# Kernel optimization log

Hardware: AMD Instinct MI355X
Metric: run time of the kernel (lower is better)

The kernel has to match this reference:

```python
import jax, jax.numpy as jnp
import numpy as np

SR = 24000          # sampling_rate
MAX_H = 60          # min(n_harmonics=100, 60)


def _interp_linear(x, T):
    """Linear upsample along axis 1, align_corners=True. x: [B, C, F] -> [B, T, F]."""
    B, C, F = x.shape
    src = jnp.arange(T, dtype=x.dtype) * ((C - 1) / (T - 1))
    i0 = jnp.clip(jnp.floor(src).astype(jnp.int32), 0, C - 2)
    frac = (src - i0.astype(x.dtype))[None, :, None]
    return x[:, i0, :] * (1.0 - frac) + x[:, i0 + 1, :] * frac


def setup_inputs() -> dict:
    key = jax.random.key(0)
    k1, k2, k3, k4, k5 = jax.random.split(key, 5)
    B, T, H, C, NF = 8, 48000, MAX_H, 100, 5
    f0 = 100.0 + 300.0 * jax.random.uniform(k1, (B, T, 1), dtype=jnp.float32)
    amplitudes = jax.random.uniform(k2, (B, T, H), dtype=jnp.float32)
    formant_freqs = 200.0 + 3300.0 * jax.random.uniform(k3, (B, C, NF), dtype=jnp.float32)
    formant_bws = 50.0 + 150.0 * jax.random.uniform(k4, (B, C, NF), dtype=jnp.float32)
    formant_amps = jax.random.uniform(k5, (B, C, NF), dtype=jnp.float32)
    initial_phase = jnp.zeros((B, 1, 1), dtype=jnp.float32)
    return {"f0": f0, "amplitudes": amplitudes, "formant_freqs": formant_freqs,
            "formant_bws": formant_bws, "formant_amps": formant_amps,
            "initial_phase": initial_phase}


def reference(f0, amplitudes, formant_freqs, formant_bws, formant_amps, initial_phase):
    B, T, _ = f0.shape
    f0 = jax.lax.stop_gradient(f0)                    # torch: f0.detach()
    voiced = (f0[..., 0] > 0).astype(f0.dtype)        # [B, T]
    phase = jnp.cumsum(2.0 * np.pi * f0 / SR, axis=1) + initial_phase  # [B, T, 1]

    ff = _interp_linear(formant_freqs, T)             # [B, T, NF]
    fb = _interp_linear(formant_bws, T)
    fa = _interp_linear(formant_amps, T)

    h = jnp.arange(1, MAX_H + 1, dtype=f0.dtype)      # [H]
    h_freq = f0 * h                                   # [B, T, H]
    nyq = (h_freq < SR / 2).astype(f0.dtype)          # [B, T, H]

    # formant resonance factor: prod over formants of (1 + amp*bw^2/((h_freq-freq)^2+bw^2))
    factor = jnp.ones_like(h_freq)
    for f in range(ff.shape[-1]):                     # NF = 5, small fixed loop
        freq = ff[:, :, f:f + 1]
        bw = fb[:, :, f:f + 1]
        amp = fa[:, :, f:f + 1]
        factor = factor * (1.0 + amp * bw * bw / ((h_freq - freq) ** 2 + bw * bw))

    osc = jnp.sin(phase * h)                          # [B, T, H]
    signal = jnp.sum(osc * amplitudes * factor * nyq, axis=-1) * voiced  # [B, T]

    final_phase = jax.lax.stop_gradient(phase[:, -1:, :] % (2.0 * np.pi))  # [B, 1, 1]
    return signal, final_phase
```

## Files before the change

kernel.cpp:

```cpp
#include <hip/hip_runtime.h>
#include <math.h>

#define SRATE   24000.0
#define NB      8
#define NT      48000
#define NH      60
#define NC      100
#define NFMT    5
#define CTS     64
#define NCH     (NT / CTS)
#define TWO_PI  6.283185307179586476925286766559

typedef float v2f __attribute__((ext_vector_type(2)));

__global__ __launch_bounds__(256) void k_partial(const float* __restrict__ f0,
                                                 double* __restrict__ part) {
    int b = blockIdx.y;
    int ch = blockIdx.x * 4 + (threadIdx.x >> 6);
    int lane = threadIdx.x & 63;
    if (ch < NCH) {
        int t = ch * CTS + lane;
        double q = (double)f0[b * NT + t];
        #pragma unroll
        for (int off = 32; off > 0; off >>= 1)
            q += __shfl_down(q, off, 64);
        if (lane == 0) part[b * NCH + ch] = q;
    }
}

__global__ __launch_bounds__(256) void k_scan(const double* __restrict__ part,
                                              double* __restrict__ offs,
                                              const float* __restrict__ initp,
                                              float* __restrict__ outf) {
    int b = blockIdx.x;
    int tid = threadIdx.x;
    int lane = tid & 63, wv = tid >> 6;
    int base = tid * 3;
    double v0 = (base     < NCH) ? part[b * NCH + base    ] : 0.0;
    double v1 = (base + 1 < NCH) ? part[b * NCH + base + 1] : 0.0;
    double v2 = (base + 2 < NCH) ? part[b * NCH + base + 2] : 0.0;
    double s = v0 + v1 + v2;
    double inc = s;
    #pragma unroll
    for (int off = 1; off < 64; off <<= 1) {
        double n = __shfl_up(inc, off, 64);
        if (lane >= off) inc += n;
    }
    __shared__ double wtot[4];
    if (lane == 63) wtot[wv] = inc;
    __syncthreads();
    double woff = 0.0;
    #pragma unroll
    for (int w = 0; w < 4; ++w)
        if (w < wv) woff += wtot[w];
    double excl = woff + inc - s;
    if (base     < NCH) offs[b * NCH + base    ] = excl;
    if (base + 1 < NCH) offs[b * NCH + base + 1] = excl + v0;
    if (base + 2 < NCH) offs[b * NCH + base + 2] = excl + v0 + v1;
    if (tid == 255) {
        double carry = woff + inc;
        double rev = carry * (1.0 / SRATE) + (double)initp[b] * (1.0 / TWO_PI);
        double fr = rev - floor(rev);
        outf[b] = (float)(fr * TWO_PI);
    }
}

__global__ __launch_bounds__(256) void k_main(const float* __restrict__ f0,
                                              const float* __restrict__ amps,
                                              const float* __restrict__ ffq,
                                              const float* __restrict__ fbw,
                                              const float* __restrict__ fam,
                                              const float* __restrict__ initp,
                                              const double* __restrict__ offs,
                                              float* __restrict__ out) {
    int b = blockIdx.y, ch = blockIdx.x;
    int wv   = threadIdx.x >> 6;
    int lane = threadIdx.x & 63;
    int g = wv * 16 + (lane >> 2);
    int j = lane & 3;
    int t_pre = ch * CTS + lane;
    int t_g   = ch * CTS + g;

    float f0v = f0[b * NT + t_pre];
    float f0s = f0v * (1.0f / 256.0f);
    float f0s_g = __shfl(f0s, g, 64);

    const float4* row = (const float4*)(amps + ((size_t)b * NT + (size_t)t_g) * NH);
    float4 q[4];
    q[0] = row[j];
    q[1] = row[4 + j];
    q[2] = make_float4(0.f, 0.f, 0.f, 0.f);
    q[3] = make_float4(0.f, 0.f, 0.f, 0.f);
    if (f0s_g * 33.0f < 46.875f) q[2] = row[8 + j];
    if (j < 3 && f0s_g * 49.0f < 46.875f) q[3] = row[12 + j];

    double inc = (double)f0v;
    #pragma unroll
    for (int off = 1; off < 64; off <<= 1) {
        double n = __shfl_up(inc, off, 64);
        if (lane >= off) inc += n;
    }
    double pre = offs[b * NCH + ch];
    double rev = (pre + inc) * (1.0 / SRATE) + (double)initp[b] * (1.0 / TWO_PI);
    float rev_f = (float)(rev - floor(rev));
    float rev_g = __shfl(rev_f, g, 64);

    double srcd = (double)t_g * (99.0 / 47999.0);
    int i0 = (int)srcd;
    if (i0 > NC - 2) i0 = NC - 2;
    float frac = (float)(srcd - (double)i0);
    float omf = 1.0f - frac;
    const float* Fq = ffq + (b * NC + i0) * NFMT;
    const float* Bw = fbw + (b * NC + i0) * NFMT;
    const float* Am = fam + (b * NC + i0) * NFMT;
    float fq_g[NFMT], c1_g[NFMT], c2_g[NFMT];
    #pragma unroll
    for (int f = 0; f < NFMT; ++f) {
        float fq = Fq[f] * omf + Fq[NFMT + f] * frac;
        float bw = Bw[f] * omf + Bw[NFMT + f] * frac;
        float am = Am[f] * omf + Am[NFMT + f] * frac;
        float bws = bw * (1.0f / 256.0f);
        fq_g[f] = fq * (1.0f / 256.0f);
        c2_g[f] = bws * bws;
        c1_g[f] = am * c2_g[f];
    }

    v2f acc2 = {0.0f, 0.0f};
    float j4 = (float)(j * 4);
    #pragma unroll
    for (int i = 0; i < 4; ++i) {
        float aq[4] = {q[i].x, q[i].y, q[i].z, q[i].w};
        #pragma unroll
        for (int p = 0; p < 2; ++p) {
            float h0 = (float)(i * 16 + p * 2 + 1) + j4;
            v2f hfl = {h0, h0 + 1.0f};
            v2f aa  = {aq[p * 2], aq[p * 2 + 1]};
            v2f hs  = f0s_g * hfl;
            v2f pN  = {1.0f, 1.0f};
            v2f pD  = {1.0f, 1.0f};
            #pragma unroll
            for (int f = 0; f < NFMT; ++f) {
                v2f d = hs - fq_g[f];
                v2f e = d * d + c2_g[f];
                pN *= (e + c1_g[f]);
                pD *= e;
            }
            v2f rp;
            rp.x = __builtin_amdgcn_rcpf(pD.x);
            rp.y = __builtin_amdgcn_rcpf(pD.y);
            v2f fac = pN * rp;
            v2f ar = rev_g * hfl;
            v2f sn;
            sn.x = __builtin_amdgcn_sinf(__builtin_amdgcn_fractf(ar.x));
            sn.y = __builtin_amdgcn_sinf(__builtin_amdgcn_fractf(ar.y));
            v2f fm;
            fm.x = (hs.x < 46.875f) ? fac.x : 0.0f;
            fm.y = (hs.y < 46.875f) ? fac.y : 0.0f;
            acc2 += (sn * aa) * fm;
        }
    }
    float acc = acc2.x + acc2.y;
    acc += __shfl_xor(acc, 1, 64);
    acc += __shfl_xor(acc, 2, 64);
    if (j == 0) {
        if (!(f0s_g > 0.0f)) acc = 0.0f;
        out[b * NT + t_g] = acc;
    }
}

extern "C" void kernel_launch(void* const* d_in, const int* in_sizes, int n_in,
                              void* d_out, int out_size, void* d_ws, size_t ws_size,
                              hipStream_t stream) {
    const float* f0    = (const float*)d_in[0];
    const float* amps  = (const float*)d_in[1];
    const float* ffq   = (const float*)d_in[2];
    const float* fbw   = (const float*)d_in[3];
    const float* fam   = (const float*)d_in[4];
    const float* initp = (const float*)d_in[5];
    float* out = (float*)d_out;

    double* part = (double*)d_ws;
    double* offs = part + NB * NCH;

    dim3 gpart((NCH + 3) / 4, NB);
    k_partial<<<gpart, 256, 0, stream>>>(f0, part);
    k_scan<<<NB, 256, 0, stream>>>(part, offs, initp, out + NB * NT);
    dim3 gmain(NCH, NB);
    k_main<<<gmain, 256, 0, stream>>>(f0, amps, ffq, fbw, fam, initp, offs, out);
}
```

Measured before the change: 40.41 us.

## Replace partial+scan kernels with single per-batch scan kernel emitting phase table

Merges the chunk-partial and scan kernels into one 1024-thread block per batch that walks the whole sequence with a carried prefix and writes a (f0, phase fraction) pair per sample. The main kernel then reads that pair directly, so it no longer runs a per-chunk double-precision shuffle scan. This drops one launch and the scan work from the main kernel. In exchange the prep kernel runs only 8 blocks serially over 12 tiles, which may be latency-bound, and it adds an extra 3 MB write/read round trip through global memory.

```diff
diff --git a/kernel.cpp b/kernel.cpp
--- a/kernel.cpp
+++ b/kernel.cpp
@@ -10,102 +10,92 @@
 #define CTS     64
 #define NCH     (NT / CTS)
 #define TWO_PI  6.283185307179586476925286766559
+#define TPB     1024
+#define TILE    (TPB * 4)
 
 typedef float v2f __attribute__((ext_vector_type(2)));
 
-__global__ __launch_bounds__(256) void k_partial(const float* __restrict__ f0,
-                                                 double* __restrict__ part) {
-    int b = blockIdx.y;
-    int ch = blockIdx.x * 4 + (threadIdx.x >> 6);
-    int lane = threadIdx.x & 63;
-    if (ch < NCH) {
-        int t = ch * CTS + lane;
-        double q = (double)f0[b * NT + t];
+__global__ __launch_bounds__(TPB) void k_prep(const float* __restrict__ f0,
+                                              const float* __restrict__ initp,
+                                              float2* __restrict__ prep,
+                                              float* __restrict__ outf) {
+    int b = blockIdx.x, tid = threadIdx.x;
+    int lane = tid & 63, wv = tid >> 6;
+    __shared__ double wsum[TPB / 64];
+    const float* fb = f0 + (size_t)b * NT;
+    double initrev = (double)initp[b] * (1.0 / TWO_PI);
+    double carry = 0.0;
+    int t0 = tid * 4;
+    float4 fv = (t0 < NT) ? *(const float4*)(fb + t0) : make_float4(0, 0, 0, 0);
+    for (int tile = 0; tile < NT; tile += TILE) {
+        int nt0 = tile + TILE + tid * 4;
+        float4 nxt = (nt0 < NT) ? *(const float4*)(fb + nt0) : make_float4(0, 0, 0, 0);
+        double p0 = fv.x, p1 = p0 + fv.y, p2 = p1 + fv.z, p3 = p2 + fv.w;
+        double inc = p3;
         #pragma unroll
-        for (int off = 32; off > 0; off >>= 1)
-            q += __shfl_down(q, off, 64);
-        if (lane == 0) part[b * NCH + ch] = q;
+        for (int off = 1; off < 64; off <<= 1) {
+            double n = __shfl_up(inc, off, 64);
+            if (lane >= off) inc += n;
+        }
+        if (lane == 63) wsum[wv] = inc;
+        __syncthreads();
+        double woff = carry, tot = 0.0;
+        #pragma unroll
+        for (int w = 0; w < TPB / 64; ++w) {
+            double v = wsum[w];
+            tot += v;
+            if (w < wv) woff += v;
+        }
+        __syncthreads();
+        int ct0 = tile + tid * 4;
+        if (ct0 < NT) {
+            double base = woff + inc - p3;
+            float4 lo, hi;
+            double r;
+            r = (base + p0) * (1.0 / SRATE) + initrev; lo.x = fv.x; lo.y = (float)(r - floor(r));
+            r = (base + p1) * (1.0 / SRATE) + initrev; lo.z = fv.y; lo.w = (float)(r - floor(r));
+            r = (base + p2) * (1.0 / SRATE) + initrev; hi.x = fv.z; hi.y = (float)(r - floor(r));
+            r = (base + p3) * (1.0 / SRATE) + initrev; hi.z = fv.w; hi.w = (float)(r - floor(r));
+            float4* pp = (float4*)(prep + (size_t)b * NT + ct0);
+            pp[0] = lo;
+            pp[1] = hi;
+        }
+        carry += tot;
+        fv = nxt;
     }
-}
-
-__global__ __launch_bounds__(256) void k_scan(const double* __restrict__ part,
-                                              double* __restrict__ offs,
-                                              const float* __restrict__ initp,
-                                              float* __restrict__ outf) {
-    int b = blockIdx.x;
-    int tid = threadIdx.x;
-    int lane = tid & 63, wv = tid >> 6;
-    int base = tid * 3;
-    double v0 = (base     < NCH) ? part[b * NCH + base    ] : 0.0;
-    double v1 = (base + 1 < NCH) ? part[b * NCH + base + 1] : 0.0;
-    double v2 = (base + 2 < NCH) ? part[b * NCH + base + 2] : 0.0;
-    double s = v0 + v1 + v2;
-    double inc = s;
-    #pragma unroll
-    for (int off = 1; off < 64; off <<= 1) {
-        double n = __shfl_up(inc, off, 64);
-        if (lane >= off) inc += n;
-    }
-    __shared__ double wtot[4];
-    if (lane == 63) wtot[wv] = inc;
-    __syncthreads();
-    double woff = 0.0;
-    #pragma unroll
-    for (int w = 0; w < 4; ++w)
-        if (w < wv) woff += wtot[w];
-    double excl = woff + inc - s;
-    if (base     < NCH) offs[b * NCH + base    ] = excl;
-    if (base + 1 < NCH) offs[b * NCH + base + 1] = excl + v0;
-    if (base + 2 < NCH) offs[b * NCH + base + 2] = excl + v0 + v1;
-    if (tid == 255) {
-        double carry = woff + inc;
-        double rev = carry * (1.0 / SRATE) + (double)initp[b] * (1.0 / TWO_PI);
+    if (tid == 0) {
+        double rev = carry * (1.0 / SRATE) + initrev;
         double fr = rev - floor(rev);
         outf[b] = (float)(fr * TWO_PI);
     }
 }
 
-__global__ __launch_bounds__(256) void k_main(const float* __restrict__ f0,
+__global__ __launch_bounds__(256) void k_main(const float2* __restrict__ prep,
                                               const float* __restrict__ amps,
                                               const float* __restrict__ ffq,
                                               const float* __restrict__ fbw,
                                               const float* __restrict__ fam,
-                                              const float* __restrict__ initp,
-                                              const double* __restrict__ offs,
                                               float* __restrict__ out) {
     int b = blockIdx.y, ch = blockIdx.x;
-    int wv   = threadIdx.x >> 6;
-    int lane = threadIdx.x & 63;
+    int tid = threadIdx.x;
+    int wv = tid >> 6, lane = tid & 63;
     int g = wv * 16 + (lane >> 2);
     int j = lane & 3;
-    int t_pre = ch * CTS + lane;
-    int t_g   = ch * CTS + g;
+    int t = ch * CTS + g;
 
-    float f0v = f0[b * NT + t_pre];
-    float f0s = f0v * (1.0f / 256.0f);
-    float f0s_g = __shfl(f0s, g, 64);
+    const float4* row = (const float4*)(amps + ((size_t)b * NT + (size_t)t) * NH);
+    float4 q0 = row[j];
+    float4 q1 = row[4 + j];
+    float2 pr = prep[(size_t)b * NT + t];
+    float f0v   = pr.x;
+    float f0s   = f0v * (1.0f / 256.0f);
+    float rev_g = pr.y;
+    float4 q2 = make_float4(0.f, 0.f, 0.f, 0.f);
+    float4 q3 = make_float4(0.f, 0.f, 0.f, 0.f);
+    if (f0s * 33.0f < 46.875f) q2 = row[8 + j];
+    if (j < 3 && f0s * 49.0f < 46.875f) q3 = row[12 + j];
 
-    const float4* row = (const float4*)(amps + ((size_t)b * NT + (size_t)t_g) * NH);
-    float4 q[4];
-    q[0] = row[j];
-    q[1] = row[4 + j];
-    q[2] = make_float4(0.f, 0.f, 0.f, 0.f);
-    q[3] = make_float4(0.f, 0.f, 0.f, 0.f);
-    if (f0s_g * 33.0f < 46.875f) q[2] = row[8 + j];
-    if (j < 3 && f0s_g * 49.0f < 46.875f) q[3] = row[12 + j];
-
-    double inc = (double)f0v;
-    #pragma unroll
-    for (int off = 1; off < 64; off <<= 1) {
-        double n = __shfl_up(inc, off, 64);
-        if (lane >= off) inc += n;
-    }
-    double pre = offs[b * NCH + ch];
-    double rev = (pre + inc) * (1.0 / SRATE) + (double)initp[b] * (1.0 / TWO_PI);
-    float rev_f = (float)(rev - floor(rev));
-    float rev_g = __shfl(rev_f, g, 64);
-
-    double srcd = (double)t_g * (99.0 / 47999.0);
+    double srcd = (double)t * (99.0 / 47999.0);
     int i0 = (int)srcd;
     if (i0 > NC - 2) i0 = NC - 2;
     float frac = (float)(srcd - (double)i0);
@@ -125,6 +115,7 @@
         c1_g[f] = am * c2_g[f];
     }
 
+    float4 q[4] = {q0, q1, q2, q3};
     v2f acc2 = {0.0f, 0.0f};
     float j4 = (float)(j * 4);
     #pragma unroll
@@ -135,7 +126,7 @@
             float h0 = (float)(i * 16 + p * 2 + 1) + j4;
             v2f hfl = {h0, h0 + 1.0f};
             v2f aa  = {aq[p * 2], aq[p * 2 + 1]};
-            v2f hs  = f0s_g * hfl;
+            v2f hs  = f0s * hfl;
             v2f pN  = {1.0f, 1.0f};
             v2f pD  = {1.0f, 1.0f};
             #pragma unroll
@@ -163,8 +154,8 @@
     acc += __shfl_xor(acc, 1, 64);
     acc += __shfl_xor(acc, 2, 64);
     if (j == 0) {
-        if (!(f0s_g > 0.0f)) acc = 0.0f;
-        out[b * NT + t_g] = acc;
+        if (!(f0v > 0.0f)) acc = 0.0f;
+        out[b * NT + t] = acc;
     }
 }
 
@@ -179,12 +170,9 @@
     const float* initp = (const float*)d_in[5];
     float* out = (float*)d_out;
 
-    double* part = (double*)d_ws;
-    double* offs = part + NB * NCH;
+    float2* prep = (float2*)d_ws;
 
-    dim3 gpart((NCH + 3) / 4, NB);
-    k_partial<<<gpart, 256, 0, stream>>>(f0, part);
-    k_scan<<<NB, 256, 0, stream>>>(part, offs, initp, out + NB * NT);
+    k_prep<<<NB, TPB, 0, stream>>>(f0, initp, prep, out + NB * NT);
     dim3 gmain(NCH, NB);
-    k_main<<<gmain, 256, 0, stream>>>(f0, amps, ffq, fbw, fam, initp, offs, out);
+    k_main<<<gmain, 256, 0, stream>>>(prep, amps, ffq, fbw, fam, out);
 }
```

Result: slower. 50.70 us (+25.5%).

## Split phase computation into separate kernel and load amplitudes unconditionally

Applied to the files above, without the earlier changes.

Moves the per-chunk double-precision prefix scan and phase fraction computation out of the main kernel into a new k_rev kernel. That kernel writes (f0, phase) float2 pairs to workspace, which k_main then reads per row. k_main now loads all amplitude float4s unconditionally, drops the Nyquist-based load skipping, and adds an occupancy hint to launch_bounds. This trades an extra kernel launch and workspace round-trip for less double-precision shuffle work and fewer registers in the hot kernel. It also fetches amplitude data that was skipped before for high harmonics.

```diff
diff --git a/kernel.cpp b/kernel.cpp
--- a/kernel.cpp
+++ b/kernel.cpp
@@ -65,47 +65,52 @@
     }
 }
 
-__global__ __launch_bounds__(256) void k_main(const float* __restrict__ f0,
-                                              const float* __restrict__ amps,
-                                              const float* __restrict__ ffq,
-                                              const float* __restrict__ fbw,
-                                              const float* __restrict__ fam,
-                                              const float* __restrict__ initp,
-                                              const double* __restrict__ offs,
-                                              float* __restrict__ out) {
-    int b = blockIdx.y, ch = blockIdx.x;
-    int wv   = threadIdx.x >> 6;
+__global__ __launch_bounds__(256) void k_rev(const float* __restrict__ f0,
+                                             const double* __restrict__ offs,
+                                             const float* __restrict__ initp,
+                                             float2* __restrict__ prep) {
+    int b = blockIdx.y;
+    int ch = blockIdx.x * 4 + (threadIdx.x >> 6);
     int lane = threadIdx.x & 63;
-    int g = wv * 16 + (lane >> 2);
-    int j = lane & 3;
-    int t_pre = ch * CTS + lane;
-    int t_g   = ch * CTS + g;
-
-    float f0v = f0[b * NT + t_pre];
-    float f0s = f0v * (1.0f / 256.0f);
-    float f0s_g = __shfl(f0s, g, 64);
-
-    const float4* row = (const float4*)(amps + ((size_t)b * NT + (size_t)t_g) * NH);
-    float4 q[4];
-    q[0] = row[j];
-    q[1] = row[4 + j];
-    q[2] = make_float4(0.f, 0.f, 0.f, 0.f);
-    q[3] = make_float4(0.f, 0.f, 0.f, 0.f);
-    if (f0s_g * 33.0f < 46.875f) q[2] = row[8 + j];
-    if (j < 3 && f0s_g * 49.0f < 46.875f) q[3] = row[12 + j];
-
+    if (ch >= NCH) return;
+    int t = ch * CTS + lane;
+    float f0v = f0[b * NT + t];
     double inc = (double)f0v;
     #pragma unroll
     for (int off = 1; off < 64; off <<= 1) {
         double n = __shfl_up(inc, off, 64);
         if (lane >= off) inc += n;
     }
-    double pre = offs[b * NCH + ch];
-    double rev = (pre + inc) * (1.0 / SRATE) + (double)initp[b] * (1.0 / TWO_PI);
+    double rev = (offs[b * NCH + ch] + inc) * (1.0 / SRATE)
+               + (double)initp[b] * (1.0 / TWO_PI);
     float rev_f = (float)(rev - floor(rev));
-    float rev_g = __shfl(rev_f, g, 64);
+    prep[(size_t)b * NT + t] = make_float2(f0v, rev_f);
+}
 
-    double srcd = (double)t_g * (99.0 / 47999.0);
+__global__ __launch_bounds__(256, 4) void k_main(const float2* __restrict__ prep,
+                                                 const float* __restrict__ amps,
+                                                 const float* __restrict__ ffq,
+                                                 const float* __restrict__ fbw,
+                                                 const float* __restrict__ fam,
+                                                 float* __restrict__ out) {
+    int b = blockIdx.y, ch = blockIdx.x;
+    int tid = threadIdx.x;
+    int wv = tid >> 6, lane = tid & 63;
+    int g = wv * 16 + (lane >> 2);
+    int j = lane & 3;
+    int t = ch * CTS + g;
+
+    const float4* row = (const float4*)(amps + ((size_t)b * NT + (size_t)t) * NH);
+    float4 q0 = row[j];
+    float4 q1 = row[4 + j];
+    float4 q2 = row[8 + j];
+    float4 q3 = (j < 3) ? row[12 + j] : make_float4(0.f, 0.f, 0.f, 0.f);
+    float2 pr = prep[(size_t)b * NT + t];
+    float f0v   = pr.x;
+    float f0s   = f0v * (1.0f / 256.0f);
+    float rev_g = pr.y;
+
+    double srcd = (double)t * (99.0 / 47999.0);
     int i0 = (int)srcd;
     if (i0 > NC - 2) i0 = NC - 2;
     float frac = (float)(srcd - (double)i0);
@@ -125,6 +130,7 @@
         c1_g[f] = am * c2_g[f];
     }
 
+    float4 q[4] = {q0, q1, q2, q3};
     v2f acc2 = {0.0f, 0.0f};
     float j4 = (float)(j * 4);
     #pragma unroll
@@ -135,7 +141,7 @@
             float h0 = (float)(i * 16 + p * 2 + 1) + j4;
             v2f hfl = {h0, h0 + 1.0f};
             v2f aa  = {aq[p * 2], aq[p * 2 + 1]};
-            v2f hs  = f0s_g * hfl;
+            v2f hs  = f0s * hfl;
             v2f pN  = {1.0f, 1.0f};
             v2f pD  = {1.0f, 1.0f};
             #pragma unroll
@@ -163,8 +169,8 @@
     acc += __shfl_xor(acc, 1, 64);
     acc += __shfl_xor(acc, 2, 64);
     if (j == 0) {
-        if (!(f0s_g > 0.0f)) acc = 0.0f;
-        out[b * NT + t_g] = acc;
+        if (!(f0v > 0.0f)) acc = 0.0f;
+        out[b * NT + t] = acc;
     }
 }
 
@@ -181,10 +187,12 @@
 
     double* part = (double*)d_ws;
     double* offs = part + NB * NCH;
+    float2* prep = (float2*)(offs + NB * NCH);
 
-    dim3 gpart((NCH + 3) / 4, NB);
-    k_partial<<<gpart, 256, 0, stream>>>(f0, part);
+    dim3 gchunk((NCH + 3) / 4, NB);
+    k_partial<<<gchunk, 256, 0, stream>>>(f0, part);
     k_scan<<<NB, 256, 0, stream>>>(part, offs, initp, out + NB * NT);
+    k_rev<<<gchunk, 256, 0, stream>>>(f0, offs, initp, prep);
     dim3 gmain(NCH, NB);
-    k_main<<<gmain, 256, 0, stream>>>(f0, amps, ffq, fbw, fam, initp, offs, out);
+    k_main<<<gmain, 256, 0, stream>>>(prep, amps, ffq, fbw, fam, out);
 }
```

After: 41.18 us. About the same (+1.9%).
